# Optimization experiments

Hardware: AMD Instinct MI355X
Metric: run time of the kernel (lower is better)

The kernel has to match this reference:

```python
import jax, jax.numpy as jnp
import numpy as np

jax.config.update("jax_enable_x64", True)

B = 16384          # batch size (rows of features)
K = 256            # num_unlabel (clusters)
EPS = 0.05         # sinkhorn epsilon
GAMMA = 5.0        # KL regularizer weight
LR = 0.1           # SGD lr for w
MOM = 0.99         # SGD momentum
N_INNER = 3        # sinkhorn iterations
N_OUTER = 10       # outer optimization iterations


def setup_inputs() -> dict:
    key = jax.random.key(0)
    features = jax.random.normal(key, (B, K), dtype=jnp.float32)
    w = jnp.ones((1, K), dtype=jnp.float32) / K  # torch Parameter init: ones/K
    return {"features": features, "w": w, "head": 0}


def _sinkhorn(logits, w):
    """SinkhornKnopp_im.forward: logits [B,K] -> Q [B,K] (float64), preds=logits64."""
    logits64 = logits.astype(jnp.float64)
    Q = jnp.exp(logits64 / EPS).T            # [K, B]
    Q = Q / jnp.sum(Q)
    K2 = jax.nn.softmax(w, axis=1).astype(jnp.float64)  # [1, K] marginal prior
    Bn = Q.shape[1]
    for _ in range(N_INNER):
        Q = Q / jnp.sum(Q, axis=1, keepdims=True)       # row normalize
        Q = Q * K2.T                                    # scale rows by prior
        Q = Q / jnp.sum(Q, axis=0, keepdims=True)       # column normalize
        Q = Q / Bn
    Q = Q * Bn
    return Q.T, logits64                                # [B, K], [B, K]


def _total_loss(w, features):
    Q, preds = _sinkhorn(features, w)
    loss = -jnp.mean(jnp.sum(Q * preds, axis=1))
    # KLDivLoss(batchmean): input = log_softmax(w).T [K,1], target = softmax(w0).T = 1/K
    logw = jax.nn.log_softmax(w, axis=1)[0]             # [K]
    t = jnp.float32(1.0 / K)
    reg = jnp.sum(t * (jnp.log(t) - logw)) / K
    return loss + GAMMA * reg.astype(jnp.float64), Q


def reference(features, w, head):
    features = jax.lax.stop_gradient(features)  # features.detach()

    def step(carry, _):
        w, buf, _ = carry
        (_, Q), g = jax.value_and_grad(_total_loss, has_aux=True)(w, features)
        # clip_grad_norm_(params, 1)
        norm = jnp.sqrt(jnp.sum(g.astype(jnp.float64) ** 2)).astype(g.dtype)
        g = g * jnp.minimum(jnp.float32(1.0), jnp.float32(1.0) / (norm + 1e-6))
        # SGD with momentum 0.99 (buf starts at 0 -> first buf = g, matching torch)
        buf = MOM * buf + g
        w = w - LR * buf
        return (w, buf, Q), None

    Q0 = jnp.zeros((features.shape[0], K), dtype=jnp.float64)
    (w_f, buf_f, Q), _ = jax.lax.scan(
        step, (w, jnp.zeros_like(w), Q0), None, length=N_OUTER
    )
    return Q  # Q from the last outer iteration (computed with pre-update w)
```

## Files before the change

kernel.cpp:

```cpp
#include <hip/hip_runtime.h>


namespace {

constexpr int KDIM = 256;
constexpr int NBLK = 256;
constexpr int ROWS = 64;
constexpr int NREP = 16;
constexpr int NPH  = 48;
constexpr float L2E20 = 28.853900817779268f;

constexpr size_t P_DBL   = 2ull * NBLK * KDIM;
constexpr size_t RES_OFF = P_DBL;
constexpr size_t RES_DBL = (size_t)NPH * NREP * KDIM;
constexpr size_t WS_DBL  = P_DBL + RES_DBL;

__device__ __forceinline__ double fast_exp_d(double x) {
  const double LOG2E  = 1.4426950408889634074;
  const double LN2_HI = 6.93147180369123816490e-01;
  const double LN2_LO = 1.90821492927058770002e-10;
  double n = rint(x * LOG2E);
  double t = fma(-n, LN2_HI, x);
  t = fma(-n, LN2_LO, t);
  double p = 2.4801587301587302e-05;
  p = fma(p, t, 1.9841269841269841e-04);
  p = fma(p, t, 1.3888888888888889e-03);
  p = fma(p, t, 8.3333333333333333e-03);
  p = fma(p, t, 4.1666666666666664e-02);
  p = fma(p, t, 1.6666666666666666e-01);
  p = fma(p, t, 0.5);
  p = fma(p, t, 1.0);
  p = fma(p, t, 1.0);
  long long ni = (long long)n;
  double s = __longlong_as_double((unsigned long long)(ni + 1023LL) << 52);
  return p * s;
}

__device__ __forceinline__ double wave_sum_d(double v) {
#pragma unroll
  for (int o = 32; o > 0; o >>= 1) v += __shfl_down(v, o);
  return v;
}
__device__ __forceinline__ double wave_max_d(double v) {
#pragma unroll
  for (int o = 32; o > 0; o >>= 1) v = fmax(v, __shfl_down(v, o));
  return v;
}

__device__ __forceinline__ double pload(const double* p) {
  return __hip_atomic_load(p, __ATOMIC_RELAXED, __HIP_MEMORY_SCOPE_AGENT);
}
__device__ __forceinline__ void pstore(double* p, double v) {
  __hip_atomic_store(p, v, __ATOMIC_RELAXED, __HIP_MEMORY_SCOPE_AGENT);
}

}

__global__ __launch_bounds__(256) void kInitWS(double* __restrict__ ws) {
  const double QN = __builtin_nan("");
  size_t gid = (size_t)blockIdx.x * 256 + threadIdx.x;
  size_t stride = (size_t)gridDim.x * 256;
  for (size_t j = gid; j < WS_DBL; j += stride) ws[j] = QN;
}

__global__ __launch_bounds__(256, 1) void sink_main(
    const float* __restrict__ feat, const float* __restrict__ w_in,
    float* __restrict__ out, double* __restrict__ ws) {
  __shared__ float  Et[ROWS * KDIM];
  __shared__ float  Ft[ROWS * KDIM];
  __shared__ double alpha[KDIM];
  __shared__ double v1s[ROWS], v2s[ROWS], v3s[ROWS];
  __shared__ double grow[ROWS], wrow[ROWS], sbr[ROWS];
  __shared__ float  mrow[ROWS];
  __shared__ double sred[8];

  const int t = threadIdx.x, bid = blockIdx.x;
  const int wv = t >> 6, lane = t & 63;
  const int b0 = bid * ROWS;
  const double QN = __builtin_nan("");

  double* P   = ws;
  double* res = ws + RES_OFF;

  auto blk_sum = [&](double v) -> double {
    v = wave_sum_d(v);
    __syncthreads();
    if (lane == 0) sred[wv] = v;
    __syncthreads();
    return sred[0] + sred[1] + sred[2] + sred[3];
  };
  auto blk_max = [&](double v) -> double {
    v = wave_max_d(v);
    __syncthreads();
    if (lane == 0) sred[wv + 4] = v;
    __syncthreads();
    return fmax(fmax(sred[4], sred[5]), fmax(sred[6], sred[7]));
  };

  auto allreduce = [&](unsigned ph, double pa) -> double {
    const int p = ph & 1;
    pstore(P + ((size_t)p * NBLK + bid) * KDIM + t, pa);
    double* e = P + ((size_t)p * NBLK + t) * KDIM + bid;
    double v;
    for (;;) {
      v = pload(e);
      if (!__builtin_isnan(v)) break;
      __builtin_amdgcn_s_sleep(1);
    }
    pstore(e, QN);
    v = wave_sum_d(v);
    __syncthreads();
    if (lane == 0) sred[wv] = v;
    __syncthreads();
    double s = sred[0] + sred[1] + sred[2] + sred[3];
    if (t < NREP) pstore(res + ((size_t)ph * NREP + t) * KDIM + bid, s);
    const double* re = res + ((size_t)ph * NREP + (bid & (NREP - 1))) * KDIM + t;
    double r;
    for (;;) {
      r = pload(re);
      if (!__builtin_isnan(r)) break;
      __builtin_amdgcn_s_sleep(1);
    }
    return r;
  };

  auto row_pass = [&](double* dstv) {
    double a0 = alpha[4 * lane + 0], a1 = alpha[4 * lane + 1];
    double a2 = alpha[4 * lane + 2], a3 = alpha[4 * lane + 3];
#pragma unroll 4
    for (int r = wv; r < ROWS; r += 4) {
      float4 e4 = ((const float4*)(Et + r * KDIM))[lane];
      double s1 = a0 * (double)e4.x + a1 * (double)e4.y +
                  a2 * (double)e4.z + a3 * (double)e4.w;
      s1 = wave_sum_d(s1);
      if (lane == 0) dstv[r] = s1;
    }
  };
  auto col_partial = [&]() -> double {
    double a = 0.0;
#pragma unroll 8
    for (int r = 0; r < ROWS; ++r) a += (double)Et[r * KDIM + t] * wrow[r];
    return a;
  };

  {
    const float4* src = (const float4*)(feat + (size_t)b0 * KDIM);
    float4* dst = (float4*)Ft;
#pragma unroll
    for (int s = 0; s < 16; ++s) dst[s * 256 + t] = src[s * 256 + t];
  }
  __syncthreads();
  for (int r = wv; r < ROWS; r += 4) {
    float4 f4 = ((const float4*)(Ft + r * KDIM))[lane];
    float m = fmaxf(fmaxf(f4.x, f4.y), fmaxf(f4.z, f4.w));
#pragma unroll
    for (int o = 32; o > 0; o >>= 1) m = fmaxf(m, __shfl_down(m, o));
    if (lane == 0) {
      mrow[r] = m;
      sbr[r] = fast_exp_d(20.0 * (double)m);
    }
  }
  __syncthreads();
  double pu0 = 0.0;
#pragma unroll 8
  for (int r = 0; r < ROWS; ++r) {
    float e = exp2f((Ft[r * KDIM + t] - mrow[r]) * L2E20);
    Et[r * KDIM + t] = e;
    pu0 += (double)e * sbr[r];
  }
  float w_t = w_in[t], buf_t = 0.0f;
  double k2_t;
  {
    double x = (double)w_t;
    double m = blk_max(x);
    double e = fast_exp_d(x - m);
    double s = blk_sum(e);
    k2_t = e / s;
  }
  unsigned ph = 0;
  double u0_t = allreduce(ph, pu0);

  for (int it = 0; it < 10; ++it) {
    double u1_t, u2_t;

    alpha[t] = k2_t / u0_t;
    __syncthreads();
    row_pass(v1s);
    __syncthreads();
    if (t < ROWS) wrow[t] = 1.0 / (16384.0 * v1s[t]);
    __syncthreads();
    {
      double pa = col_partial();
      ++ph; u1_t = allreduce(ph, pa);
    }

    alpha[t] = k2_t / u1_t;
    __syncthreads();
    row_pass(v2s);
    __syncthreads();
    if (t < ROWS) wrow[t] = 1.0 / (16384.0 * v2s[t]);
    __syncthreads();
    {
      double pa = col_partial();
      ++ph; u2_t = allreduce(ph, pa);
    }

    if (it == 9) {
      alpha[t] = k2_t / u2_t;
      __syncthreads();
      row_pass(v3s);
      __syncthreads();
      if (t < ROWS) wrow[t] = 1.0 / v3s[t];
      __syncthreads();
      double a3 = alpha[t];
#pragma unroll 4
      for (int r = 0; r < ROWS; ++r)
        out[(size_t)(b0 + r) * KDIM + t] =
            (float)(a3 * (double)Et[r * KDIM + t] * wrow[r]);
      return;
    }

    alpha[t] = k2_t / u2_t;
    __syncthreads();
    {
      double a0 = alpha[4 * lane + 0], a1 = alpha[4 * lane + 1];
      double a2 = alpha[4 * lane + 2], a3 = alpha[4 * lane + 3];
#pragma unroll 2
      for (int r = wv; r < ROWS; r += 4) {
        float4 e4 = ((const float4*)(Et + r * KDIM))[lane];
        float4 f4 = ((const float4*)(Ft + r * KDIM))[lane];
        double p0 = a0 * (double)e4.x, p1 = a1 * (double)e4.y;
        double p2 = a2 * (double)e4.z, p3 = a3 * (double)e4.w;
        double s1 = p0 + p1 + p2 + p3;
        double s2 = p0 * (double)f4.x + p1 * (double)f4.y +
                    p2 * (double)f4.z + p3 * (double)f4.w;
        s1 = wave_sum_d(s1);
        s2 = wave_sum_d(s2);
        if (lane == 0) {
          v3s[r] = s1;
          grow[r] = s2 / (16384.0 * s1 * s1);
        }
      }
    }
    __syncthreads();
    if (t < ROWS) wrow[t] = -1.0 / (16384.0 * v3s[t]);
    __syncthreads();
    double gsum_t;
    {
      double ac1 = 0.0, ac2 = 0.0;
#pragma unroll 8
      for (int r = 0; r < ROWS; ++r) {
        double ed = (double)Et[r * KDIM + t];
        ac1 += ed * (double)Ft[r * KDIM + t] * wrow[r];
        ac2 += ed * grow[r];
      }
      ++ph; gsum_t = allreduce(ph, ac1 + ac2);
    }

    alpha[t] = -gsum_t * k2_t / (u2_t * u2_t);
    __syncthreads();
    row_pass(grow);
    __syncthreads();
    if (t < ROWS) wrow[t] = -grow[t] / (16384.0 * v2s[t] * v2s[t]);
    __syncthreads();
    double ga2_t;
    {
      double pa = col_partial();
      ++ph; ga2_t = allreduce(ph, pa);
    }

    alpha[t] = -ga2_t * k2_t / (u1_t * u1_t);
    __syncthreads();
    row_pass(grow);
    __syncthreads();
    if (t < ROWS) wrow[t] = -grow[t] / (16384.0 * v1s[t] * v1s[t]);
    __syncthreads();
    double ga1_t;
    {
      double pa = col_partial();
      ++ph; ga1_t = allreduce(ph, pa);
    }

    {
      double gk2 = gsum_t / u2_t + ga2_t / u1_t + ga1_t / u0_t;
      double dot = blk_sum(k2_t * gk2);
      double gw = k2_t * (gk2 - dot) + 5.0 * (k2_t / 256.0 - 1.0 / 65536.0);
      double n2 = blk_sum(gw * gw);
      float normf = (float)sqrt(n2);
      float sc = fminf(1.0f, 1.0f / (normf + 1e-6f));
      float g = (float)gw * sc;
      buf_t = 0.99f * buf_t + g;
      w_t = w_t - 0.1f * buf_t;
      double x = (double)w_t;
      double m = blk_max(x);
      double e = fast_exp_d(x - m);
      double s = blk_sum(e);
      k2_t = e / s;
    }
  }
}

extern "C" void kernel_launch(void* const* d_in, const int* in_sizes, int n_in,
                              void* d_out, int out_size, void* d_ws,
                              size_t ws_size, hipStream_t stream) {
  (void)in_sizes; (void)n_in; (void)out_size; (void)ws_size;
  const float* feat = (const float*)d_in[0];
  const float* w_in = (const float*)d_in[1];
  float* out = (float*)d_out;
  double* ws = (double*)d_ws;

  kInitWS<<<128, 256, 0, stream>>>(ws);
  sink_main<<<NBLK, 256, 0, stream>>>(feat, w_in, out, ws);
}
```

Before: 659.4 us.

## Replace NaN-flag transpose allreduce with slotted atomic-add accumulation and counters

The cross-block allreduce previously used a NaN-sentinel transpose exchange: each block stored a partial vector, polled for the others' partials, summed them and published replicated results. It now atomically adds its partial into one of 16 slot accumulators per phase, bumps a per-slot counter, waits until every slot counter reaches 16, then sums the 16 slots. This is meant to cut polling traffic and the second exchange round. In exchange it relies on float atomic-add contention and the ordering between the data atomics and the relaxed counter increment. Atomic accumulation order also makes the sums nondeterministic.

```diff
diff --git a/kernel.cpp b/kernel.cpp
--- a/kernel.cpp
+++ b/kernel.cpp
@@ -6,14 +6,13 @@
 constexpr int KDIM = 256;
 constexpr int NBLK = 256;
 constexpr int ROWS = 64;
-constexpr int NREP = 16;
+constexpr int NSLOT = 16;
 constexpr int NPH  = 48;
 constexpr float L2E20 = 28.853900817779268f;
 
-constexpr size_t P_DBL   = 2ull * NBLK * KDIM;
-constexpr size_t RES_OFF = P_DBL;
-constexpr size_t RES_DBL = (size_t)NPH * NREP * KDIM;
-constexpr size_t WS_DBL  = P_DBL + RES_DBL;
+constexpr size_t ACC_DBL = (size_t)NPH * NSLOT * KDIM;
+constexpr size_t CNT_OFF_DBL = ACC_DBL;
+constexpr int CNT_U32 = NPH * 16 * 16;
 
 __device__ __forceinline__ double fast_exp_d(double x) {
   const double LOG2E  = 1.4426950408889634074;
@@ -50,17 +49,18 @@
 __device__ __forceinline__ double pload(const double* p) {
   return __hip_atomic_load(p, __ATOMIC_RELAXED, __HIP_MEMORY_SCOPE_AGENT);
 }
-__device__ __forceinline__ void pstore(double* p, double v) {
-  __hip_atomic_store(p, v, __ATOMIC_RELAXED, __HIP_MEMORY_SCOPE_AGENT);
+__device__ __forceinline__ unsigned aload(const unsigned* p) {
+  return __hip_atomic_load(p, __ATOMIC_RELAXED, __HIP_MEMORY_SCOPE_AGENT);
 }
 
 }
 
 __global__ __launch_bounds__(256) void kInitWS(double* __restrict__ ws) {
-  const double QN = __builtin_nan("");
   size_t gid = (size_t)blockIdx.x * 256 + threadIdx.x;
   size_t stride = (size_t)gridDim.x * 256;
-  for (size_t j = gid; j < WS_DBL; j += stride) ws[j] = QN;
+  for (size_t j = gid; j < ACC_DBL; j += stride) ws[j] = 0.0;
+  unsigned* c = (unsigned*)(ws + CNT_OFF_DBL);
+  for (size_t j = gid; j < (size_t)CNT_U32; j += stride) c[j] = 0u;
 }
 
 __global__ __launch_bounds__(256, 1) void sink_main(
@@ -77,10 +77,10 @@
   const int t = threadIdx.x, bid = blockIdx.x;
   const int wv = t >> 6, lane = t & 63;
   const int b0 = bid * ROWS;
-  const double QN = __builtin_nan("");
-
-  double* P   = ws;
-  double* res = ws + RES_OFF;
+  const int slot = bid & (NSLOT - 1);
+
+  double* acc = ws;
+  unsigned* cnt = (unsigned*)(ws + CNT_OFF_DBL);
 
   auto blk_sum = [&](double v) -> double {
     v = wave_sum_d(v);
@@ -98,30 +98,27 @@
   };
 
   auto allreduce = [&](unsigned ph, double pa) -> double {
-    const int p = ph & 1;
-    pstore(P + ((size_t)p * NBLK + bid) * KDIM + t, pa);
-    double* e = P + ((size_t)p * NBLK + t) * KDIM + bid;
-    double v;
-    for (;;) {
-      v = pload(e);
-      if (!__builtin_isnan(v)) break;
-      __builtin_amdgcn_s_sleep(1);
-    }
-    pstore(e, QN);
-    v = wave_sum_d(v);
-    __syncthreads();
-    if (lane == 0) sred[wv] = v;
-    __syncthreads();
-    double s = sred[0] + sred[1] + sred[2] + sred[3];
-    if (t < NREP) pstore(res + ((size_t)ph * NREP + t) * KDIM + bid, s);
-    const double* re = res + ((size_t)ph * NREP + (bid & (NREP - 1))) * KDIM + t;
-    double r;
-    for (;;) {
-      r = pload(re);
-      if (!__builtin_isnan(r)) break;
-      __builtin_amdgcn_s_sleep(1);
-    }
-    return r;
+    double* A = acc + (size_t)ph * NSLOT * KDIM;
+    unsafeAtomicAdd(A + (size_t)slot * KDIM + t, pa);
+    asm volatile("s_waitcnt vmcnt(0)" ::: "memory");
+    __syncthreads();
+    if (t == 0)
+      __hip_atomic_fetch_add(cnt + ((size_t)ph * 16 + slot) * 16, 1u,
+                             __ATOMIC_RELAXED, __HIP_MEMORY_SCOPE_AGENT);
+    if (t < NSLOT) {
+      const unsigned* c = cnt + ((size_t)ph * 16 + t) * 16;
+      unsigned v = aload(c);
+      while (v < 16u) {
+        __builtin_amdgcn_s_sleep(4);
+        v = aload(c);
+      }
+    }
+    __syncthreads();
+    const double* A0 = A + t;
+    double tot = 0.0;
+#pragma unroll
+    for (int s = 0; s < NSLOT; ++s) tot += pload(A0 + (size_t)s * KDIM);
+    return tot;
   };
 
   auto row_pass = [&](double* dstv) {
```

After: 633.2 us. 1.04x faster.
